# Performance work log

Hardware: AMD Instinct MI355X
Metric: run time of the kernel (lower is better)

## Reference

```python
import jax, jax.numpy as jnp
import numpy as np

B, T, N, F, O = 4, 8192, 64, 16, 32  # batch, timesteps, vertices, in_feat, out_feat


def setup_inputs() -> dict:
    key = jax.random.key(0)
    ks = jax.random.split(key, 8)
    return {
        "x": jax.random.normal(ks[0], (B, T, N * F), dtype=jnp.float32),
        "adj": jax.random.uniform(ks[1], (N, N), dtype=jnp.float32),
        "W1": jax.random.normal(ks[2], (T,), dtype=jnp.float32) / np.sqrt(T).astype(np.float32),
        "W2": jax.random.normal(ks[3], (F, T), dtype=jnp.float32) / np.sqrt(F).astype(np.float32),
        "W3": jax.random.normal(ks[4], (F,), dtype=jnp.float32) / np.sqrt(F).astype(np.float32),
        "bs": jax.random.normal(ks[5], (1, N, N), dtype=jnp.float32) * 0.02,
        "Vs": jax.random.normal(ks[6], (N, N), dtype=jnp.float32) * 0.02,
        "conv_w": jax.random.normal(ks[7], (O, N * F, 3), dtype=jnp.float32) * 0.02,
    }


def reference(x, adj, W1, W2, W3, bs, Vs, conv_w):
    bz, t, _ = x.shape
    x4 = x.reshape(bz, t, N, F)
    xp = jnp.transpose(x4, (0, 2, 3, 1))  # (B, N, F, T)

    # Spatial attention: S in (B, N, N)
    lhs = jnp.einsum('bnft,t->bnf', xp, W1) @ W2          # (B, N, T)
    rhs = jnp.einsum('f,bnft->bnt', W3, xp)               # (B, N, T)
    product = jnp.einsum('bnt,bmt->bnm', lhs, rhs)        # (B, N, N)
    S = jnp.einsum('nm,bmk->bnk', Vs, jax.nn.sigmoid(product + bs))
    S = jax.nn.softmax(S, axis=1)

    # Apply attention over the vertex dim
    xr = jnp.transpose(x4, (0, 1, 3, 2)).reshape(bz, t * F, N)  # (B, T*F, N)
    xm = jnp.einsum('bpn,bnm->bpm', xr, S)                      # (B, T*F, N)
    xf = jnp.transpose(xm.reshape(bz, t, F, N), (0, 2, 1, 3))   # (B, F, T, N)

    # einsum 'bftn,nn->bftn' == scale by diagonal of adj
    xf = xf * jnp.diagonal(adj)                                 # broadcast over N

    xo = jnp.transpose(xf, (0, 2, 3, 1)).reshape(bz, t, N * F)  # (B, T, N*F)

    # Conv1d(kernel=3, padding=1, no bias), channels-last
    out = jax.lax.conv_general_dilated(
        xo, conv_w,
        window_strides=(1,), padding=((1, 1),),
        dimension_numbers=('NWC', 'OIW', 'NWC'))
    return out  # (B, T, O)
```

## Files before the change

### kernel.cpp

```cpp
#include <hip/hip_runtime.h>
#include <hip/hip_bf16.h>

#define B_ 4
#define T_ 8192
#define N_ 64
#define F_ 16
#define O_ 32

typedef _Float16 half8_t __attribute__((ext_vector_type(8)));
typedef float float4_t __attribute__((ext_vector_type(4)));

#define WS_A1G  0
#define WS_SSC  32768
#define WS_WFT  98304
#define WS_P    884736

#define TB_ 64

__global__ __launch_bounds__(256) void kA2(const float* __restrict__ x,
                                           const float* __restrict__ W1,
                                           const float* __restrict__ W2,
                                           const float* __restrict__ W3,
                                           float* __restrict__ P) {
    __shared__ float w2s[16][TB_ + 1];
    __shared__ float w1s[TB_];
    const int b    = blockIdx.x >> 7;
    const int tile = blockIdx.x & 127;
    const int t0   = tile * TB_;
    const int tid  = threadIdx.x;
    const int fq   = tid & 3;

    for (int i = tid; i < 16 * TB_; i += 256) {
        const int f = i >> 6, r = i & 63;
        w2s[f][r] = W2[f * T_ + t0 + r];
    }
    if (tid < TB_) w1s[tid] = W1[t0 + tid];
    __syncthreads();

    float w3v[4];
#pragma unroll
    for (int j = 0; j < 4; ++j) w3v[j] = W3[fq * 4 + j];

    const float* xbase = x + ((size_t)b * T_ + t0) * 1024 + tid * 4;
    float4_t accA = {0.f, 0.f, 0.f, 0.f};
    float4_t accG = {0.f, 0.f, 0.f, 0.f};

#pragma unroll 4
    for (int r = 0; r < TB_; ++r) {
        float4_t xv = *(const float4_t*)(xbase + (size_t)r * 1024);
        float v = xv[0] * w3v[0] + xv[1] * w3v[1] + xv[2] * w3v[2] + xv[3] * w3v[3];
        v += __shfl_xor(v, 1);
        v += __shfl_xor(v, 2);
        const float w1r = w1s[r];
#pragma unroll
        for (int j = 0; j < 4; ++j) {
            accA[j] += w1r * xv[j];
            accG[j] += w2s[fq * 4 + j][r] * v;
        }
    }

    float* pb = P + (size_t)blockIdx.x * 2048 + tid * 4;
    *(float4_t*)pb          = accA;
    *(float4_t*)(pb + 1024) = accG;
}

__global__ __launch_bounds__(256) void kR(const float* __restrict__ P,
                                          float* __restrict__ A1G) {
    const int b   = blockIdx.x >> 3;
    const int seg = blockIdx.x & 7;
    const int tid = threadIdx.x;
    const int o4  = tid & 63;
    const int g   = tid >> 6;

    const float* base = P + (size_t)b * 128 * 2048 + seg * 256 + o4 * 4;
    float4_t s = {0.f, 0.f, 0.f, 0.f};
#pragma unroll 4
    for (int tt = 0; tt < 32; ++tt) {
        float4_t v = *(const float4_t*)(base + (size_t)(g * 32 + tt) * 2048);
        s += v;
    }

    __shared__ float4_t red[4][64];
    red[g][o4] = s;
    __syncthreads();
    if (tid < 64) {
        float4_t t = red[0][tid] + red[1][tid] + red[2][tid] + red[3][tid];
        *(float4_t*)(A1G + (size_t)b * 2048 + seg * 256 + tid * 4) = t;
    }
}

__global__ __launch_bounds__(256) void kC(const float* __restrict__ A1G,
                                          const float* __restrict__ bs,
                                          const float* __restrict__ Vs,
                                          const float* __restrict__ adj,
                                          float* __restrict__ Ssc) {
    const int b = blockIdx.x;
    __shared__ float a1[64][17], g[64][17];
    __shared__ float sig[64][64];
    __shared__ float vs[64][64];
    __shared__ float redmx[4][64];
    __shared__ float redsm[4][64];
    const int tid = threadIdx.x;

    for (int i = tid; i < 1024; i += 256) {
        a1[i >> 4][i & 15] = A1G[b * 2048 + i];
        g [i >> 4][i & 15] = A1G[b * 2048 + 1024 + i];
    }
    for (int i = tid; i < 4096; i += 256) vs[i >> 6][i & 63] = Vs[i];
    __syncthreads();

#pragma unroll
    for (int i = 0; i < 16; ++i) {
        const int e = tid + 256 * i, r = e >> 6, c = e & 63;
        float p = 0.f;
#pragma unroll
        for (int f = 0; f < 16; ++f) p += a1[r][f] * g[c][f];
        p += bs[e];
        sig[r][c] = 1.f / (1.f + __expf(-p));
    }
    __syncthreads();

    const int gw = tid >> 6;
    const int c  = tid & 63;
    const int r0 = gw * 16;

    float sc_[64];
#pragma unroll
    for (int m = 0; m < 64; ++m) sc_[m] = sig[m][c];

    float acc[16];
#pragma unroll
    for (int rl = 0; rl < 16; ++rl) {
        const float4_t* vr = (const float4_t*)&vs[r0 + rl][0];
        float sA = 0.f, sB = 0.f, sC = 0.f, sD = 0.f;
#pragma unroll
        for (int m4 = 0; m4 < 4; ++m4) {
            float4_t v0 = vr[m4];
            float4_t v1 = vr[m4 + 4];
            float4_t v2 = vr[m4 + 8];
            float4_t v3 = vr[m4 + 12];
#pragma unroll
            for (int j = 0; j < 4; ++j) {
                sA += v0[j] * sc_[m4 * 4 + j];
                sB += v1[j] * sc_[16 + m4 * 4 + j];
                sC += v2[j] * sc_[32 + m4 * 4 + j];
                sD += v3[j] * sc_[48 + m4 * 4 + j];
            }
        }
        acc[rl] = (sA + sB) + (sC + sD);
    }

    float pmax = -1e30f;
#pragma unroll
    for (int rl = 0; rl < 16; ++rl) pmax = fmaxf(pmax, acc[rl]);
    redmx[gw][c] = pmax;
    __syncthreads();
    const float mx = fmaxf(fmaxf(redmx[0][c], redmx[1][c]),
                           fmaxf(redmx[2][c], redmx[3][c]));

    float psum = 0.f;
#pragma unroll
    for (int rl = 0; rl < 16; ++rl) {
        acc[rl] = __expf(acc[rl] - mx);
        psum += acc[rl];
    }
    redsm[gw][c] = psum;
    __syncthreads();
    const float sum = (redsm[0][c] + redsm[1][c]) + (redsm[2][c] + redsm[3][c]);
    const float scl = adj[c * 64 + c] / sum;

#pragma unroll
    for (int rl = 0; rl < 16; ++rl)
        Ssc[b * 4096 + (r0 + rl) * 64 + c] = acc[rl] * scl;
}

__global__ __launch_bounds__(256) void kD(const float* __restrict__ Ssc,
                                          const float* __restrict__ conv_w,
                                          _Float16* __restrict__ Wft) {
    const int b = blockIdx.x >> 5, o = blockIdx.x & 31;
    __shared__ float ssc[4096];
    __shared__ float cw[3072];
    const int tid = threadIdx.x;
    for (int i = tid; i < 4096; i += 256) ssc[i] = Ssc[b * 4096 + i];
    for (int i = tid; i < 3072; i += 256) cw[i] = conv_w[o * 3072 + i];
    __syncthreads();

#pragma unroll
    for (int i = 0; i < 12; ++i) {
        const int e = tid + 256 * i;
        const int k = e >> 10, rem = e & 1023, m = rem >> 4, f = rem & 15;
        float s = 0.f;
#pragma unroll
        for (int n = 0; n < 64; ++n) s += cw[(n * 16 + f) * 3 + k] * ssc[m * 64 + n];
        Wft[(size_t)(b * 32 + o) * 3072 + e] = (_Float16)s;
    }
}

__global__ __launch_bounds__(256) void kE(const float* __restrict__ x,
                                          const _Float16* __restrict__ Wft,
                                          float* __restrict__ out) {
    const int b    = blockIdx.x >> 7;
    const int tile = blockIdx.x & 127;
    const int wave = threadIdx.x >> 6;
    const int lane = threadIdx.x & 63;
    const int q = lane >> 4, l = lane & 15;
    const int t0 = tile * 64 + wave * 16;

    const _Float16* wb0 = Wft + (size_t)(b * 32 + l) * 3072;
    const _Float16* wb1 = wb0 + 16 * 3072;
    const float* xb = x + (size_t)b * T_ * 1024;

    float4_t acc0 = {0.f, 0.f, 0.f, 0.f};
    float4_t acc1 = {0.f, 0.f, 0.f, 0.f};

#pragma unroll 4
    for (int kk = 0; kk < 96; ++kk) {
        const int K  = kk * 32;
        const int kc = K >> 10;
        const int c0 = (K & 1023) + q * 8;
        const int row = t0 + l + kc - 1;
        const bool valid = (unsigned)row < (unsigned)T_;
        const int rc = valid ? row : 0;
        const float sc = valid ? 1.f : 0.f;

        const float* ap = xb + (size_t)rc * 1024 + c0;
        float4_t a0 = *(const float4_t*)ap;
        float4_t a1 = *(const float4_t*)(ap + 4);

        half8_t af;
        af[0] = (_Float16)(a0[0] * sc); af[1] = (_Float16)(a0[1] * sc);
        af[2] = (_Float16)(a0[2] * sc); af[3] = (_Float16)(a0[3] * sc);
        af[4] = (_Float16)(a1[0] * sc); af[5] = (_Float16)(a1[1] * sc);
        af[6] = (_Float16)(a1[2] * sc); af[7] = (_Float16)(a1[3] * sc);

        half8_t bf0 = *(const half8_t*)(wb0 + K + q * 8);
        half8_t bf1 = *(const half8_t*)(wb1 + K + q * 8);

        acc0 = __builtin_amdgcn_mfma_f32_16x16x32_f16(af, bf0, acc0, 0, 0, 0);
        acc1 = __builtin_amdgcn_mfma_f32_16x16x32_f16(af, bf1, acc1, 0, 0, 0);
    }

#pragma unroll
    for (int rg = 0; rg < 4; ++rg) {
        const int t = t0 + q * 4 + rg;
        float* op = out + ((size_t)b * T_ + t) * 32;
        op[l]      = acc0[rg];
        op[16 + l] = acc1[rg];
    }
}

extern "C" void kernel_launch(void* const* d_in, const int* in_sizes, int n_in,
                              void* d_out, int out_size, void* d_ws, size_t ws_size,
                              hipStream_t stream) {
    const float* x      = (const float*)d_in[0];
    const float* adj    = (const float*)d_in[1];
    const float* W1     = (const float*)d_in[2];
    const float* W2     = (const float*)d_in[3];
    const float* W3     = (const float*)d_in[4];
    const float* bs     = (const float*)d_in[5];
    const float* Vs     = (const float*)d_in[6];
    const float* conv_w = (const float*)d_in[7];
    float* out = (float*)d_out;

    char* ws = (char*)d_ws;
    float*    A1G = (float*)(ws + WS_A1G);
    float*    Ssc = (float*)(ws + WS_SSC);
    _Float16* Wft = (_Float16*)(ws + WS_WFT);
    float*    P   = (float*)(ws + WS_P);

    kA2<<<B_ * (T_ / TB_), 256, 0, stream>>>(x, W1, W2, W3, P);
    kR <<<B_ * 8,          256, 0, stream>>>(P, A1G);
    kC <<<B_,              256, 0, stream>>>(A1G, bs, Vs, adj, Ssc);
    kD <<<B_ * O_,         256, 0, stream>>>(Ssc, conv_w, Wft);
    kE <<<B_ * (T_ / 64),  256, 0, stream>>>(x, Wft, out);
}
```

Before: 324.9 us.

## Emit padded fp16 copy of x in reduction pass and read it in conv GEMM

The first pass over x now also writes an fp16 copy of x into workspace, with a zero row of padding at each sequence edge. The final MFMA conv kernel then loads half8 vectors straight from that copy, which halves its read traffic and removes per-element conversion and boundary checks. The first pass is also retiled to 32 timesteps per block, doubling its block count and the partial-sum reduction length. The cost is an extra ~67MB write, and the new path runs only when the workspace is large enough, otherwise the fp32 kernel is used.

```diff
diff --git a/kernel.cpp b/kernel.cpp
--- a/kernel.cpp
+++ b/kernel.cpp
@@ -8,30 +8,34 @@
 #define O_ 32
 
 typedef _Float16 half8_t __attribute__((ext_vector_type(8)));
+typedef _Float16 half4_t __attribute__((ext_vector_type(4)));
 typedef float float4_t __attribute__((ext_vector_type(4)));
 
 #define WS_A1G  0
 #define WS_SSC  32768
 #define WS_WFT  98304
-#define WS_P    884736
-
-#define TB_ 64
+#define WS_P    524288
+#define WS_XH   9437184
+#define XH_BYTES ((size_t)B_ * (T_ + 2) * 1024 * sizeof(_Float16))
+
+#define TB_ 32
 
 __global__ __launch_bounds__(256) void kA2(const float* __restrict__ x,
                                            const float* __restrict__ W1,
                                            const float* __restrict__ W2,
                                            const float* __restrict__ W3,
-                                           float* __restrict__ P) {
+                                           float* __restrict__ P,
+                                           _Float16* __restrict__ xh) {
     __shared__ float w2s[16][TB_ + 1];
     __shared__ float w1s[TB_];
-    const int b    = blockIdx.x >> 7;
-    const int tile = blockIdx.x & 127;
+    const int b    = blockIdx.x >> 8;
+    const int tile = blockIdx.x & 255;
     const int t0   = tile * TB_;
     const int tid  = threadIdx.x;
     const int fq   = tid & 3;
 
     for (int i = tid; i < 16 * TB_; i += 256) {
-        const int f = i >> 6, r = i & 63;
+        const int f = i >> 5, r = i & 31;
         w2s[f][r] = W2[f * T_ + t0 + r];
     }
     if (tid < TB_) w1s[tid] = W1[t0 + tid];
@@ -42,12 +46,20 @@
     for (int j = 0; j < 4; ++j) w3v[j] = W3[fq * 4 + j];
 
     const float* xbase = x + ((size_t)b * T_ + t0) * 1024 + tid * 4;
+    _Float16* xrow = xh ? (xh + ((size_t)b * (T_ + 2) + (t0 + 1)) * 1024 + tid * 4)
+                        : (_Float16*)nullptr;
     float4_t accA = {0.f, 0.f, 0.f, 0.f};
     float4_t accG = {0.f, 0.f, 0.f, 0.f};
 
-#pragma unroll 4
+#pragma unroll 8
     for (int r = 0; r < TB_; ++r) {
         float4_t xv = *(const float4_t*)(xbase + (size_t)r * 1024);
+        if (xh) {
+            half4_t hv;
+            hv[0] = (_Float16)xv[0]; hv[1] = (_Float16)xv[1];
+            hv[2] = (_Float16)xv[2]; hv[3] = (_Float16)xv[3];
+            *(half4_t*)(xrow + (size_t)r * 1024) = hv;
+        }
         float v = xv[0] * w3v[0] + xv[1] * w3v[1] + xv[2] * w3v[2] + xv[3] * w3v[3];
         v += __shfl_xor(v, 1);
         v += __shfl_xor(v, 2);
@@ -57,6 +69,14 @@
             accA[j] += w1r * xv[j];
             accG[j] += w2s[fq * 4 + j][r] * v;
         }
+    }
+
+    if (xh) {
+        half4_t z = {(_Float16)0.f, (_Float16)0.f, (_Float16)0.f, (_Float16)0.f};
+        if (tile == 0)
+            *(half4_t*)(xh + (size_t)b * (T_ + 2) * 1024 + tid * 4) = z;
+        if (tile == 255)
+            *(half4_t*)(xh + ((size_t)b * (T_ + 2) + T_ + 1) * 1024 + tid * 4) = z;
     }
 
     float* pb = P + (size_t)blockIdx.x * 2048 + tid * 4;
@@ -72,11 +92,11 @@
     const int o4  = tid & 63;
     const int g   = tid >> 6;
 
-    const float* base = P + (size_t)b * 128 * 2048 + seg * 256 + o4 * 4;
+    const float* base = P + (size_t)b * 256 * 2048 + seg * 256 + o4 * 4;
     float4_t s = {0.f, 0.f, 0.f, 0.f};
 #pragma unroll 4
-    for (int tt = 0; tt < 32; ++tt) {
-        float4_t v = *(const float4_t*)(base + (size_t)(g * 32 + tt) * 2048);
+    for (int tt = 0; tt < 64; ++tt) {
+        float4_t v = *(const float4_t*)(base + (size_t)(g * 64 + tt) * 2048);
         s += v;
     }
 
@@ -196,9 +216,49 @@
     }
 }
 
-__global__ __launch_bounds__(256) void kE(const float* __restrict__ x,
-                                          const _Float16* __restrict__ Wft,
-                                          float* __restrict__ out) {
+__global__ __launch_bounds__(256) void kE16(const _Float16* __restrict__ xh,
+                                            const _Float16* __restrict__ Wft,
+                                            float* __restrict__ out) {
+    const int b    = blockIdx.x >> 7;
+    const int tile = blockIdx.x & 127;
+    const int wave = threadIdx.x >> 6;
+    const int lane = threadIdx.x & 63;
+    const int q = lane >> 4, l = lane & 15;
+    const int t0 = tile * 64 + wave * 16;
+
+    const _Float16* wb0 = Wft + (size_t)(b * 32 + l) * 3072;
+    const _Float16* wb1 = wb0 + 16 * 3072;
+    const _Float16* xb = xh + ((size_t)b * (T_ + 2) + (t0 + l)) * 1024 + q * 8;
+
+    float4_t acc0 = {0.f, 0.f, 0.f, 0.f};
+    float4_t acc1 = {0.f, 0.f, 0.f, 0.f};
+
+#pragma unroll 8
+    for (int kk = 0; kk < 96; ++kk) {
+        const int K  = kk * 32;
+        const int kc = K >> 10;
+        const int c0 = K & 1023;
+
+        half8_t af  = *(const half8_t*)(xb + (size_t)kc * 1024 + c0);
+        half8_t bf0 = *(const half8_t*)(wb0 + K + q * 8);
+        half8_t bf1 = *(const half8_t*)(wb1 + K + q * 8);
+
+        acc0 = __builtin_amdgcn_mfma_f32_16x16x32_f16(af, bf0, acc0, 0, 0, 0);
+        acc1 = __builtin_amdgcn_mfma_f32_16x16x32_f16(af, bf1, acc1, 0, 0, 0);
+    }
+
+#pragma unroll
+    for (int rg = 0; rg < 4; ++rg) {
+        const int t = t0 + q * 4 + rg;
+        float* op = out + ((size_t)b * T_ + t) * 32;
+        op[l]      = acc0[rg];
+        op[16 + l] = acc1[rg];
+    }
+}
+
+__global__ __launch_bounds__(256) void kE32(const float* __restrict__ x,
+                                            const _Float16* __restrict__ Wft,
+                                            float* __restrict__ out) {
     const int b    = blockIdx.x >> 7;
     const int tile = blockIdx.x & 127;
     const int wave = threadIdx.x >> 6;
@@ -268,9 +328,13 @@
     _Float16* Wft = (_Float16*)(ws + WS_WFT);
     float*    P   = (float*)(ws + WS_P);
 
-    kA2<<<B_ * (T_ / TB_), 256, 0, stream>>>(x, W1, W2, W3, P);
+    const bool use16 = ws_size >= (size_t)WS_XH + XH_BYTES;
+    _Float16* xh = use16 ? (_Float16*)(ws + WS_XH) : (_Float16*)nullptr;
+
+    kA2<<<B_ * (T_ / TB_), 256, 0, stream>>>(x, W1, W2, W3, P, xh);
     kR <<<B_ * 8,          256, 0, stream>>>(P, A1G);
     kC <<<B_,              256, 0, stream>>>(A1G, bs, Vs, adj, Ssc);
     kD <<<B_ * O_,         256, 0, stream>>>(Ssc, conv_w, Wft);
-    kE <<<B_ * (T_ / 64),  256, 0, stream>>>(x, Wft, out);
-}
+    if (use16) kE16<<<B_ * (T_ / 64), 256, 0, stream>>>(xh, Wft, out);
+    else       kE32<<<B_ * (T_ / 64), 256, 0, stream>>>(x, Wft, out);
+}
```

Result: no change. 319.1 us (-1.8%).

## Emit padded fp16 copy of x in first pass and feed MFMA kernel from it

Applied to the files above, without the earlier changes.

The reduction kernel now also writes x as fp16 into a workspace buffer with zero rows at both ends of each batch, so the conv GEMM kernel reads half the bytes and needs no boundary checks or per-element conversion. The conv weight buffer is relaid so each lane's B fragment is one contiguous load per k-step. The first pass tile size is halved to launch more blocks, and the partial-sum reducer is adjusted to match. The trade-off is an extra 64MB fp16 write in the first pass plus the larger workspace, in exchange for cheaper reads in the GEMM.

```diff
diff --git a/kernel.cpp b/kernel.cpp
--- a/kernel.cpp
+++ b/kernel.cpp
@@ -8,30 +8,34 @@
 #define O_ 32
 
 typedef _Float16 half8_t __attribute__((ext_vector_type(8)));
+typedef _Float16 half4_t __attribute__((ext_vector_type(4)));
 typedef float float4_t __attribute__((ext_vector_type(4)));
 
 #define WS_A1G  0
 #define WS_SSC  32768
 #define WS_WFT  98304
 #define WS_P    884736
-
-#define TB_ 64
+#define WS_XH   18874368
+#define XH_BYTES ((size_t)B_ * (T_ + 2) * 1024 * sizeof(_Float16))
+
+#define TB_ 32
 
 __global__ __launch_bounds__(256) void kA2(const float* __restrict__ x,
                                            const float* __restrict__ W1,
                                            const float* __restrict__ W2,
                                            const float* __restrict__ W3,
-                                           float* __restrict__ P) {
+                                           float* __restrict__ P,
+                                           _Float16* __restrict__ xh) {
     __shared__ float w2s[16][TB_ + 1];
     __shared__ float w1s[TB_];
-    const int b    = blockIdx.x >> 7;
-    const int tile = blockIdx.x & 127;
+    const int b    = blockIdx.x >> 8;
+    const int tile = blockIdx.x & 255;
     const int t0   = tile * TB_;
     const int tid  = threadIdx.x;
     const int fq   = tid & 3;
 
     for (int i = tid; i < 16 * TB_; i += 256) {
-        const int f = i >> 6, r = i & 63;
+        const int f = i >> 5, r = i & 31;
         w2s[f][r] = W2[f * T_ + t0 + r];
     }
     if (tid < TB_) w1s[tid] = W1[t0 + tid];
@@ -42,12 +46,18 @@
     for (int j = 0; j < 4; ++j) w3v[j] = W3[fq * 4 + j];
 
     const float* xbase = x + ((size_t)b * T_ + t0) * 1024 + tid * 4;
+    _Float16* xhb = xh + ((size_t)b * (T_ + 2) + t0 + 1) * 1024 + tid * 4;
     float4_t accA = {0.f, 0.f, 0.f, 0.f};
     float4_t accG = {0.f, 0.f, 0.f, 0.f};
 
-#pragma unroll 4
+#pragma unroll 8
     for (int r = 0; r < TB_; ++r) {
         float4_t xv = *(const float4_t*)(xbase + (size_t)r * 1024);
+        half4_t hv;
+        hv[0] = (_Float16)xv[0]; hv[1] = (_Float16)xv[1];
+        hv[2] = (_Float16)xv[2]; hv[3] = (_Float16)xv[3];
+        *(half4_t*)(xhb + (size_t)r * 1024) = hv;
+
         float v = xv[0] * w3v[0] + xv[1] * w3v[1] + xv[2] * w3v[2] + xv[3] * w3v[3];
         v += __shfl_xor(v, 1);
         v += __shfl_xor(v, 2);
@@ -59,6 +69,14 @@
         }
     }
 
+    {
+        half4_t z = {(_Float16)0.f, (_Float16)0.f, (_Float16)0.f, (_Float16)0.f};
+        if (tile == 0)
+            *(half4_t*)(xh + (size_t)b * (T_ + 2) * 1024 + tid * 4) = z;
+        if (tile == 255)
+            *(half4_t*)(xh + ((size_t)b * (T_ + 2) + T_ + 1) * 1024 + tid * 4) = z;
+    }
+
     float* pb = P + (size_t)blockIdx.x * 2048 + tid * 4;
     *(float4_t*)pb          = accA;
     *(float4_t*)(pb + 1024) = accG;
@@ -66,13 +84,13 @@
 
 __global__ __launch_bounds__(256) void kR(const float* __restrict__ P,
                                           float* __restrict__ A1G) {
-    const int b   = blockIdx.x >> 3;
-    const int seg = blockIdx.x & 7;
+    const int b   = blockIdx.x >> 4;
+    const int seg = blockIdx.x & 15;
     const int tid = threadIdx.x;
-    const int o4  = tid & 63;
-    const int g   = tid >> 6;
-
-    const float* base = P + (size_t)b * 128 * 2048 + seg * 256 + o4 * 4;
+    const int o4  = tid & 31;
+    const int g   = tid >> 5;
+
+    const float* base = P + (size_t)b * 256 * 2048 + seg * 128 + o4 * 4;
     float4_t s = {0.f, 0.f, 0.f, 0.f};
 #pragma unroll 4
     for (int tt = 0; tt < 32; ++tt) {
@@ -80,12 +98,14 @@
         s += v;
     }
 
-    __shared__ float4_t red[4][64];
+    __shared__ float4_t red[8][32];
     red[g][o4] = s;
     __syncthreads();
-    if (tid < 64) {
-        float4_t t = red[0][tid] + red[1][tid] + red[2][tid] + red[3][tid];
-        *(float4_t*)(A1G + (size_t)b * 2048 + seg * 256 + tid * 4) = t;
+    if (tid < 32) {
+        float4_t t = {0.f, 0.f, 0.f, 0.f};
+#pragma unroll
+        for (int gg = 0; gg < 8; ++gg) t += red[gg][tid];
+        *(float4_t*)(A1G + (size_t)b * 2048 + seg * 128 + tid * 4) = t;
     }
 }
 
@@ -185,6 +205,8 @@
     for (int i = tid; i < 3072; i += 256) cw[i] = conv_w[o * 3072 + i];
     __syncthreads();
 
+    const size_t obase = (size_t)(b * 2 + (o >> 4)) * 49152 + (size_t)(o & 15) * 8;
+
 #pragma unroll
     for (int i = 0; i < 12; ++i) {
         const int e = tid + 256 * i;
@@ -192,13 +214,15 @@
         float s = 0.f;
 #pragma unroll
         for (int n = 0; n < 64; ++n) s += cw[(n * 16 + f) * 3 + k] * ssc[m * 64 + n];
-        Wft[(size_t)(b * 32 + o) * 3072 + e] = (_Float16)s;
-    }
-}
-
-__global__ __launch_bounds__(256) void kE(const float* __restrict__ x,
-                                          const _Float16* __restrict__ Wft,
-                                          float* __restrict__ out) {
+        const size_t wi = obase + (size_t)(e >> 5) * 512
+                        + (size_t)(((e >> 3) & 3) * 16) * 8 + (e & 7);
+        Wft[wi] = (_Float16)s;
+    }
+}
+
+__global__ __launch_bounds__(256) void kE16(const _Float16* __restrict__ xh,
+                                            const _Float16* __restrict__ Wft,
+                                            float* __restrict__ out) {
     const int b    = blockIdx.x >> 7;
     const int tile = blockIdx.x & 127;
     const int wave = threadIdx.x >> 6;
@@ -206,35 +230,21 @@
     const int q = lane >> 4, l = lane & 15;
     const int t0 = tile * 64 + wave * 16;
 
-    const _Float16* wb0 = Wft + (size_t)(b * 32 + l) * 3072;
-    const _Float16* wb1 = wb0 + 16 * 3072;
-    const float* xb = x + (size_t)b * T_ * 1024;
+    const _Float16* wb0 = Wft + (size_t)(b * 2)     * 49152 + lane * 8;
+    const _Float16* wb1 = Wft + (size_t)(b * 2 + 1) * 49152 + lane * 8;
+    const _Float16* xb = xh + ((size_t)b * (T_ + 2) + (t0 + l)) * 1024 + q * 8;
 
     float4_t acc0 = {0.f, 0.f, 0.f, 0.f};
     float4_t acc1 = {0.f, 0.f, 0.f, 0.f};
 
 #pragma unroll 4
     for (int kk = 0; kk < 96; ++kk) {
-        const int K  = kk * 32;
-        const int kc = K >> 10;
-        const int c0 = (K & 1023) + q * 8;
-        const int row = t0 + l + kc - 1;
-        const bool valid = (unsigned)row < (unsigned)T_;
-        const int rc = valid ? row : 0;
-        const float sc = valid ? 1.f : 0.f;
-
-        const float* ap = xb + (size_t)rc * 1024 + c0;
-        float4_t a0 = *(const float4_t*)ap;
-        float4_t a1 = *(const float4_t*)(ap + 4);
-
-        half8_t af;
-        af[0] = (_Float16)(a0[0] * sc); af[1] = (_Float16)(a0[1] * sc);
-        af[2] = (_Float16)(a0[2] * sc); af[3] = (_Float16)(a0[3] * sc);
-        af[4] = (_Float16)(a1[0] * sc); af[5] = (_Float16)(a1[1] * sc);
-        af[6] = (_Float16)(a1[2] * sc); af[7] = (_Float16)(a1[3] * sc);
-
-        half8_t bf0 = *(const half8_t*)(wb0 + K + q * 8);
-        half8_t bf1 = *(const half8_t*)(wb1 + K + q * 8);
+        const int kc = kk >> 5;
+        const int c0 = (kk * 32) & 1023;
+
+        half8_t af  = *(const half8_t*)(xb + (size_t)kc * 1024 + c0);
+        half8_t bf0 = *(const half8_t*)(wb0 + (size_t)kk * 512);
+        half8_t bf1 = *(const half8_t*)(wb1 + (size_t)kk * 512);
 
         acc0 = __builtin_amdgcn_mfma_f32_16x16x32_f16(af, bf0, acc0, 0, 0, 0);
         acc1 = __builtin_amdgcn_mfma_f32_16x16x32_f16(af, bf1, acc1, 0, 0, 0);
@@ -267,10 +277,11 @@
     float*    Ssc = (float*)(ws + WS_SSC);
     _Float16* Wft = (_Float16*)(ws + WS_WFT);
     float*    P   = (float*)(ws + WS_P);
-
-    kA2<<<B_ * (T_ / TB_), 256, 0, stream>>>(x, W1, W2, W3, P);
-    kR <<<B_ * 8,          256, 0, stream>>>(P, A1G);
-    kC <<<B_,              256, 0, stream>>>(A1G, bs, Vs, adj, Ssc);
-    kD <<<B_ * O_,         256, 0, stream>>>(Ssc, conv_w, Wft);
-    kE <<<B_ * (T_ / 64),  256, 0, stream>>>(x, Wft, out);
-}
+    _Float16* xh  = (_Float16*)(ws + WS_XH);
+
+    kA2 <<<B_ * (T_ / TB_), 256, 0, stream>>>(x, W1, W2, W3, P, xh);
+    kR  <<<B_ * 16,         256, 0, stream>>>(P, A1G);
+    kC  <<<B_,              256, 0, stream>>>(A1G, bs, Vs, adj, Ssc);
+    kD  <<<B_ * O_,         256, 0, stream>>>(Ssc, conv_w, Wft);
+    kE16<<<B_ * (T_ / 64),  256, 0, stream>>>(xh, Wft, out);
+}
```

Result: faster. 288.6 us (-11.2%).
